# Kernel tuning notes

Measured on AMD Instinct MI355X. Metric: run time of the kernel, lower is better.

Reference implementation:

```python
import jax, jax.numpy as jnp
import numpy as np

N_NODES = 2048
N_EDGES = 32768
NEG_SLOPE = 0.01  # torch F.leaky_relu default used in DGL GAT tutorial


def gat_layer(h, W, a, src, dst):
    """Multi-head GAT layer (DGL tutorial math), concat merge.
    h: [N, F_in], W: [H, F_in, D], a: [H, 2D], src/dst: [E].
    Returns [N, H*D].
    """
    n = h.shape[0]
    D = W.shape[2]
    z = jnp.einsum('ni,hio->nho', h, W)                      # [N,H,D]
    a_src, a_dst = a[:, :D], a[:, D:]
    s_src = jnp.einsum('nhd,hd->nh', z, a_src)               # [N,H]
    s_dst = jnp.einsum('nhd,hd->nh', z, a_dst)               # [N,H]
    e = jax.nn.leaky_relu(s_src[src] + s_dst[dst], NEG_SLOPE)  # [E,H]
    # softmax over incoming edges per destination node
    e_max = jax.ops.segment_max(e, dst, num_segments=n)      # [N,H]
    ex = jnp.exp(e - e_max[dst])                             # [E,H]
    denom = jax.ops.segment_sum(ex, dst, num_segments=n)     # [N,H]
    alpha = ex / denom[dst]                                  # [E,H]
    msg = alpha[:, :, None] * z[src]                         # [E,H,D]
    out = jax.ops.segment_sum(msg, dst, num_segments=n)      # [N,H,D]
    return out.reshape(n, -1)


def setup_inputs() -> dict:
    key = jax.random.key(0)
    ks = jax.random.split(key, 12)

    def w(k, h, i, o):
        return jax.random.normal(k, (h, i, o), jnp.float32) / np.float32(np.sqrt(i))

    def av(k, h, o):
        return jax.random.normal(k, (h, 2 * o), jnp.float32) / np.float32(np.sqrt(2 * o))

    feat = jax.random.normal(ks[0], (N_NODES, 512), jnp.float32)
    W1 = w(ks[1], 16, 512, 512);   a1 = av(ks[2], 16, 512)
    W2 = w(ks[3], 16, 8192, 512);  a2 = av(ks[4], 16, 512)
    W3 = w(ks[5], 16, 8192, 512);  a3 = av(ks[6], 16, 512)
    W4 = w(ks[7], 1, 8192, 512);   a4 = av(ks[8], 1, 512)
    src = jax.random.randint(ks[9], (N_EDGES,), 0, N_NODES, jnp.int32)
    # guarantee every node has at least one incoming edge (no empty softmax)
    dst_rand = jax.random.randint(ks[10], (N_EDGES - N_NODES,), 0, N_NODES, jnp.int32)
    dst = jnp.concatenate([jnp.arange(N_NODES, dtype=jnp.int32), dst_rand])
    return dict(feat=feat, W1=W1, a1=a1, W2=W2, a2=a2, W3=W3, a3=a3,
                W4=W4, a4=a4, src=src, dst=dst)


def reference(feat, W1, a1, W2, a2, W3, a3, W4, a4, src, dst):
    x = gat_layer(feat, W1, a1, src, dst)   # [N, 8192]
    x = gat_layer(x, W2, a2, src, dst)      # [N, 8192]
    x = gat_layer(x, W3, a3, src, dst)      # [N, 8192]
    x = gat_layer(x, W4, a4, src, dst)      # [N, 512]
    return x
```

## Files before the change

kernel.cpp:

```cpp
#include <hip/hip_runtime.h>
#include <hip/hip_bf16.h>
#include <stdint.h>

#define N_NODES 2048
#define N_EDGES 32768

using short8  = __attribute__((ext_vector_type(8))) short;
using floatx4 = __attribute__((ext_vector_type(4))) float;

__device__ __forceinline__ unsigned short f2bf(float f) {
  unsigned u = __float_as_uint(f);
  unsigned r = (u + 0x7fffu + ((u >> 16) & 1u)) >> 16;
  return (unsigned short)r;
}
__device__ __forceinline__ float wave_sum(float v) {
  #pragma unroll
  for (int o = 32; o > 0; o >>= 1) v += __shfl_xor(v, o);
  return v;
}
__device__ __forceinline__ float wave_max(float v) {
  #pragma unroll
  for (int o = 32; o > 0; o >>= 1) v = fmaxf(v, __shfl_xor(v, o));
  return v;
}

__global__ __launch_bounds__(256) void cast_feat(
    const float* __restrict__ in, unsigned short* __restrict__ out, int n4)
{
  int i = blockIdx.x * 256 + threadIdx.x;
  if (i < n4) {
    float4 v = ((const float4*)in)[i];
    ushort4 o;
    o.x = f2bf(v.x); o.y = f2bf(v.y); o.z = f2bf(v.z); o.w = f2bf(v.w);
    ((ushort4*)out)[i] = o;
  }
}

__global__ __launch_bounds__(256) void transpose_w(
    const float* __restrict__ W, unsigned short* __restrict__ Wt, int Fin)
{
  __shared__ unsigned short tile[64][68];
  const int h  = blockIdx.z;
  const int k0 = blockIdx.x * 64;
  const int d0 = blockIdx.y * 64;
  const int t  = threadIdx.x;
  const float*    Wh  = W  + (size_t)h * Fin * 512;
  unsigned short* Wth = Wt + (size_t)h * 512 * Fin;

  const int dl = (t & 15) * 4;
  const int kr = t >> 4;
  #pragma unroll
  for (int p = 0; p < 4; ++p) {
    int k = kr + p * 16;
    float4 v = *(const float4*)(Wh + (size_t)(k0 + k) * 512 + d0 + dl);
    ushort4 b;
    b.x = f2bf(v.x); b.y = f2bf(v.y); b.z = f2bf(v.z); b.w = f2bf(v.w);
    *(ushort4*)&tile[k][dl] = b;
  }
  __syncthreads();
  const int kl = (t & 15) * 4;
  const int dr = t >> 4;
  #pragma unroll
  for (int p = 0; p < 4; ++p) {
    int d = dr + p * 16;
    ushort4 v;
    v.x = tile[kl + 0][d];
    v.y = tile[kl + 1][d];
    v.z = tile[kl + 2][d];
    v.w = tile[kl + 3][d];
    *(ushort4*)(Wth + (size_t)(d0 + d) * Fin + k0 + kl) = v;
  }
}

#define GLDS(g, l) __builtin_amdgcn_global_load_lds(                       \
    (const __attribute__((address_space(1))) void*)(g),                    \
    (__attribute__((address_space(3))) void*)(l), 16, 0, 0)

__global__ __launch_bounds__(512, 2) void gemm8(
    const unsigned short* __restrict__ A,
    const unsigned short* __restrict__ Bt,
    float* __restrict__ C, int K, int ldc, int colbase)
{
  __shared__ __align__(16) unsigned short lds_buf[4][16384];

  const int tid  = threadIdx.x;
  const int w    = tid >> 6;
  const int lane = tid & 63;
  const int l16  = lane & 15;
  const int quad = lane >> 4;
  const int warp_m = w >> 2;
  const int warp_n = w & 3;

  const int nwg = gridDim.x;
  const int cpx = nwg >> 3;
  const int wg  = (blockIdx.x & 7) * cpx + (blockIdx.x >> 3);
  const int mt  = wg & 7;
  const int nt  = wg >> 3;

  const int NT = K >> 5;

  const int srow = lane >> 2;
  const int gch  = ((lane & 3) ^ ((lane >> 3) & 3)) * 8;
  const unsigned short* pa0 = A  + (size_t)(mt * 256 + w * 32 + srow) * K + gch;
  const unsigned short* pa1 = pa0 + (size_t)16 * K;
  const unsigned short* pb0 = Bt + (size_t)(nt * 256 + w * 32 + srow) * K + gch;
  const unsigned short* pb1 = pb0 + (size_t)16 * K;

  const int fA   = (l16 >> 1) & 3;
  const int cswz = (quad ^ fA) * 8;
  const int a_off = (warp_m * 128 + l16) * 32 + cswz;
  const int b_off = 8192 + (warp_n * 64 + l16) * 32 + cswz;

  floatx4 acc[8][4];
  #pragma unroll
  for (int i = 0; i < 8; ++i)
    #pragma unroll
    for (int j = 0; j < 4; ++j)
      acc[i][j] = (floatx4){0.f, 0.f, 0.f, 0.f};

  {
    unsigned short* dA0 = &lds_buf[0][w * 1024];
    unsigned short* dB0 = &lds_buf[0][8192 + w * 1024];
    GLDS(pa0, dA0); GLDS(pa1, dA0 + 512);
    GLDS(pb0, dB0); GLDS(pb1, dB0 + 512);
    unsigned short* dA1 = &lds_buf[1][w * 1024];
    unsigned short* dB1 = &lds_buf[1][8192 + w * 1024];
    GLDS(pa0 + 32, dA1); GLDS(pa1 + 32, dA1 + 512);
    GLDS(pb0 + 32, dB1); GLDS(pb1 + 32, dB1 + 512);
  }
  asm volatile("s_waitcnt vmcnt(4)");
  __builtin_amdgcn_s_barrier();
  __builtin_amdgcn_sched_barrier(0);

  const unsigned short* sa0 = pa0 + 64;
  const unsigned short* sa1 = pa1 + 64;
  const unsigned short* sb0 = pb0 + 64;
  const unsigned short* sb1 = pb1 + 64;

  for (int t = 0; t < NT; ++t) {
    const int s  = t & 3;
    const int s2 = (t + 2) & 3;
    const unsigned short* sl  = &lds_buf[s][0];
    const unsigned short* rdA = sl + a_off;
    const unsigned short* rdB = sl + b_off;
    const bool st = (t + 2) < NT;

    short8 af[4], bf4[4];
    #pragma unroll
    for (int mi = 0; mi < 4; ++mi)
      af[mi] = *(const short8*)(rdA + mi * 512);
    #pragma unroll
    for (int ni = 0; ni < 4; ++ni)
      bf4[ni] = *(const short8*)(rdB + ni * 512);
    if (st) {
      unsigned short* dA = &lds_buf[s2][w * 1024];
      GLDS(sa0, dA); GLDS(sa1, dA + 512);
    }
    __builtin_amdgcn_sched_barrier(0);
    __builtin_amdgcn_s_barrier();
    asm volatile("s_waitcnt lgkmcnt(0)");
    __builtin_amdgcn_sched_barrier(0);
    __builtin_amdgcn_s_setprio(1);
    #pragma unroll
    for (int mi = 0; mi < 4; ++mi)
      #pragma unroll
      for (int ni = 0; ni < 4; ++ni)
        acc[mi][ni] = __builtin_amdgcn_mfma_f32_16x16x32_bf16(
            af[mi], bf4[ni], acc[mi][ni], 0, 0, 0);
    __builtin_amdgcn_s_setprio(0);
    __builtin_amdgcn_sched_barrier(0);
    __builtin_amdgcn_s_barrier();
    __builtin_amdgcn_sched_barrier(0);

    short8 ag[4];
    #pragma unroll
    for (int mi = 0; mi < 4; ++mi)
      ag[mi] = *(const short8*)(rdA + (mi + 4) * 512);
    if (st) {
      unsigned short* dB = &lds_buf[s2][8192 + w * 1024];
      GLDS(sb0, dB); GLDS(sb1, dB + 512);
    }
    __builtin_amdgcn_sched_barrier(0);
    __builtin_amdgcn_s_barrier();
    asm volatile("s_waitcnt lgkmcnt(0)");
    __builtin_amdgcn_sched_barrier(0);
    __builtin_amdgcn_s_setprio(1);
    #pragma unroll
    for (int mi = 0; mi < 4; ++mi)
      #pragma unroll
      for (int ni = 0; ni < 4; ++ni)
        acc[mi + 4][ni] = __builtin_amdgcn_mfma_f32_16x16x32_bf16(
            ag[mi], bf4[ni], acc[mi + 4][ni], 0, 0, 0);
    __builtin_amdgcn_s_setprio(0);
    __builtin_amdgcn_sched_barrier(0);
    if (st) asm volatile("s_waitcnt vmcnt(4)");
    else    asm volatile("s_waitcnt vmcnt(0)");
    __builtin_amdgcn_s_barrier();
    __builtin_amdgcn_sched_barrier(0);

    sa0 += 32; sa1 += 32; sb0 += 32; sb1 += 32;
  }

  float* Cb = C + (size_t)(mt * 256 + warp_m * 128) * ldc
                + colbase + nt * 256 + warp_n * 64;
  #pragma unroll
  for (int mi = 0; mi < 8; ++mi)
    #pragma unroll
    for (int ni = 0; ni < 4; ++ni)
      #pragma unroll
      for (int r = 0; r < 4; ++r) {
        int row = mi * 16 + quad * 4 + r;
        int col = ni * 16 + l16;
        Cb[(size_t)row * ldc + col] = acc[mi][ni][r];
      }
}

__global__ __launch_bounds__(256) void gemm_bt(
    const unsigned short* __restrict__ A,
    const unsigned short* __restrict__ Bt,
    float* __restrict__ C, int K, int HD, int h0, int klen)
{
  __shared__ unsigned short As[128 * 32];
  __shared__ unsigned short Bs[128 * 32];
  const int tid  = threadIdx.x;
  const int w    = tid >> 6;
  const int lane = tid & 63;
  const int mt   = blockIdx.x;
  const int nt   = blockIdx.y;
  const int hloc = nt >> 2;
  const int nloc = (nt & 3) << 7;
  const int kstart = blockIdx.z * klen;

  const unsigned short* Ab = A  + (size_t)mt * 128 * K;
  const unsigned short* Bb = Bt + (size_t)hloc * 512 * K + (size_t)nloc * K;

  const int srow = lane >> 2;
  const int scol = (lane & 3) << 3;
  const unsigned short* ga = Ab + (size_t)(w * 32 + srow) * K + scol + kstart;
  const unsigned short* gb = Bb + (size_t)(w * 32 + srow) * K + scol + kstart;

  floatx4 acc[4][4];
  #pragma unroll
  for (int i = 0; i < 4; ++i)
    #pragma unroll
    for (int j = 0; j < 4; ++j)
      acc[i][j] = (floatx4){0.f, 0.f, 0.f, 0.f};

  const int quad = lane >> 4;
  const int l16  = lane & 15;
  const int wm   = (w >> 1) << 6;
  const int wn   = (w & 1) << 6;

  for (int kb = 0; kb < klen; kb += 32) {
    __builtin_amdgcn_global_load_lds(
        (const __attribute__((address_space(1))) void*)ga,
        (__attribute__((address_space(3))) void*)&As[w * 1024], 16, 0, 0);
    __builtin_amdgcn_global_load_lds(
        (const __attribute__((address_space(1))) void*)(ga + (size_t)16 * K),
        (__attribute__((address_space(3))) void*)&As[w * 1024 + 512], 16, 0, 0);
    __builtin_amdgcn_global_load_lds(
        (const __attribute__((address_space(1))) void*)gb,
        (__attribute__((address_space(3))) void*)&Bs[w * 1024], 16, 0, 0);
    __builtin_amdgcn_global_load_lds(
        (const __attribute__((address_space(1))) void*)(gb + (size_t)16 * K),
        (__attribute__((address_space(3))) void*)&Bs[w * 1024 + 512], 16, 0, 0);
    ga += 32; gb += 32;
    __syncthreads();

    short8 af[4], bfr[4];
    #pragma unroll
    for (int mi = 0; mi < 4; ++mi)
      af[mi] = *(const short8*)&As[(wm + mi * 16 + l16) * 32 + quad * 8];
    #pragma unroll
    for (int ni = 0; ni < 4; ++ni)
      bfr[ni] = *(const short8*)&Bs[(wn + ni * 16 + l16) * 32 + quad * 8];
    #pragma unroll
    for (int mi = 0; mi < 4; ++mi)
      #pragma unroll
      for (int ni = 0; ni < 4; ++ni)
        acc[mi][ni] = __builtin_amdgcn_mfma_f32_16x16x32_bf16(
            af[mi], bfr[ni], acc[mi][ni], 0, 0, 0);
    __syncthreads();
  }

  float* Cb = C + (size_t)(mt * 128) * HD + (h0 + hloc) * 512 + nloc;
  if (gridDim.z > 1) {
    #pragma unroll
    for (int mi = 0; mi < 4; ++mi)
      #pragma unroll
      for (int ni = 0; ni < 4; ++ni)
        #pragma unroll
        for (int r = 0; r < 4; ++r) {
          int row = wm + mi * 16 + quad * 4 + r;
          int col = wn + ni * 16 + l16;
          atomicAdd(&Cb[(size_t)row * HD + col], acc[mi][ni][r]);
        }
  } else {
    #pragma unroll
    for (int mi = 0; mi < 4; ++mi)
      #pragma unroll
      for (int ni = 0; ni < 4; ++ni)
        #pragma unroll
        for (int r = 0; r < 4; ++r) {
          int row = wm + mi * 16 + quad * 4 + r;
          int col = wn + ni * 16 + l16;
          Cb[(size_t)row * HD + col] = acc[mi][ni][r];
        }
  }
}

__global__ __launch_bounds__(64) void sdot_kernel(
    const float* __restrict__ z, const float* __restrict__ a,
    float* __restrict__ ssrc, float* __restrict__ sdst, int H)
{
  const int idx  = blockIdx.x;
  const int n    = idx / H;
  const int h    = idx % H;
  const int lane = threadIdx.x;
  const float4* zr = (const float4*)(z + (size_t)n * H * 512 + h * 512 + lane * 8);
  float4 z0 = zr[0], z1 = zr[1];
  const float4* as = (const float4*)(a + (size_t)h * 1024 + lane * 8);
  const float4* ad = (const float4*)(a + (size_t)h * 1024 + 512 + lane * 8);
  float4 a0 = as[0], a1 = as[1];
  float4 b0 = ad[0], b1 = ad[1];
  float s1 = z0.x*a0.x + z0.y*a0.y + z0.z*a0.z + z0.w*a0.w
           + z1.x*a1.x + z1.y*a1.y + z1.z*a1.z + z1.w*a1.w;
  float s2 = z0.x*b0.x + z0.y*b0.y + z0.z*b0.z + z0.w*b0.w
           + z1.x*b1.x + z1.y*b1.y + z1.z*b1.z + z1.w*b1.w;
  s1 = wave_sum(s1);
  s2 = wave_sum(s2);
  if (lane == 0) { ssrc[idx] = s1; sdst[idx] = s2; }
}

__global__ void count_k(const int* __restrict__ dst, int* __restrict__ cnt) {
  int e = blockIdx.x * 256 + threadIdx.x;
  if (e < N_EDGES) atomicAdd(&cnt[dst[e]], 1);
}

__global__ __launch_bounds__(256) void scan_k(
    const int* __restrict__ cnt, int* __restrict__ offs, int* __restrict__ cur)
{
  __shared__ int part[256];
  int t = threadIdx.x;
  int loc[8]; int s = 0;
  #pragma unroll
  for (int j = 0; j < 8; ++j) { loc[j] = s; s += cnt[t * 8 + j]; }
  part[t] = s;
  __syncthreads();
  for (int d = 1; d < 256; d <<= 1) {
    int v = (t >= d) ? part[t - d] : 0;
    __syncthreads();
    part[t] += v;
    __syncthreads();
  }
  int base = (t == 0) ? 0 : part[t - 1];
  #pragma unroll
  for (int j = 0; j < 8; ++j) {
    int o = base + loc[j];
    offs[t * 8 + j] = o;
    cur[t * 8 + j]  = o;
  }
  if (t == 255) offs[2048] = part[255];
}

__global__ void scatter_k(const int* __restrict__ dst, const int* __restrict__ srcv,
                          int* __restrict__ cur, int* __restrict__ esrc) {
  int e = blockIdx.x * 256 + threadIdx.x;
  if (e < N_EDGES) {
    int p = atomicAdd(&cur[dst[e]], 1);
    esrc[p] = srcv[e];
  }
}

__global__ __launch_bounds__(64) void attn_agg(
    const float* __restrict__ z, const float* __restrict__ ssrc,
    const float* __restrict__ sdst, const int* __restrict__ offs,
    const int* __restrict__ esrc, unsigned short* __restrict__ outb,
    float* __restrict__ outf, int H)
{
  const int n = blockIdx.x, h = blockIdx.y, lane = threadIdx.x;
  const int s0 = offs[n], s1 = offs[n + 1];
  const float sd = sdst[n * H + h];

  float m = -3e38f;
  for (int i = s0 + lane; i < s1; i += 64) {
    float s = ssrc[esrc[i] * H + h] + sd;
    s = (s > 0.f) ? s : s * 0.01f;
    m = fmaxf(m, s);
  }
  m = wave_max(m);

  float den = 0.f;
  for (int i = s0 + lane; i < s1; i += 64) {
    float s = ssrc[esrc[i] * H + h] + sd;
    s = (s > 0.f) ? s : s * 0.01f;
    den += __expf(s - m);
  }
  den = wave_sum(den);
  const float inv = 1.f / den;

  float acc[8] = {0.f, 0.f, 0.f, 0.f, 0.f, 0.f, 0.f, 0.f};
  const float* zb = z + (size_t)h * 512 + lane * 8;
  for (int i = s0; i < s1; ++i) {
    int se = esrc[i];
    float s = ssrc[se * H + h] + sd;
    s = (s > 0.f) ? s : s * 0.01f;
    float alpha = __expf(s - m) * inv;
    const float4* zr = (const float4*)(zb + (size_t)se * H * 512);
    float4 q0 = zr[0], q1 = zr[1];
    acc[0] += alpha * q0.x; acc[1] += alpha * q0.y;
    acc[2] += alpha * q0.z; acc[3] += alpha * q0.w;
    acc[4] += alpha * q1.x; acc[5] += alpha * q1.y;
    acc[6] += alpha * q1.z; acc[7] += alpha * q1.w;
  }

  const size_t base = (size_t)n * H * 512 + h * 512 + lane * 8;
  if (outf) {
    float4 o0 = {acc[0], acc[1], acc[2], acc[3]};
    float4 o1 = {acc[4], acc[5], acc[6], acc[7]};
    *(float4*)(outf + base)     = o0;
    *(float4*)(outf + base + 4) = o1;
  } else {
    uint4 pk;
    pk.x = (unsigned)f2bf(acc[0]) | ((unsigned)f2bf(acc[1]) << 16);
    pk.y = (unsigned)f2bf(acc[2]) | ((unsigned)f2bf(acc[3]) << 16);
    pk.z = (unsigned)f2bf(acc[4]) | ((unsigned)f2bf(acc[5]) << 16);
    pk.w = (unsigned)f2bf(acc[6]) | ((unsigned)f2bf(acc[7]) << 16);
    *(uint4*)(outb + base) = pk;
  }
}

extern "C" void kernel_launch(void* const* d_in, const int* in_sizes, int n_in,
                              void* d_out, int out_size, void* d_ws, size_t ws_size,
                              hipStream_t stream)
{
  (void)in_sizes; (void)n_in; (void)out_size;
  const float* feat = (const float*)d_in[0];
  const float* W1   = (const float*)d_in[1];
  const float* a1   = (const float*)d_in[2];
  const float* W2   = (const float*)d_in[3];
  const float* a2   = (const float*)d_in[4];
  const float* W3   = (const float*)d_in[5];
  const float* a3   = (const float*)d_in[6];
  const float* W4   = (const float*)d_in[7];
  const float* a4   = (const float*)d_in[8];
  const int* src = (const int*)d_in[9];
  const int* dst = (const int*)d_in[10];
  float* out = (float*)d_out;

  const size_t WT16 = (size_t)16 * 512 * 8192 * 2;
  const size_t WT8  = WT16 / 2;
  const size_t ZSZ  = (size_t)N_NODES * 16 * 512 * 4;
  const size_t XSZ  = (size_t)N_NODES * 8192 * 2;
  const size_t X0SZ = (size_t)N_NODES * 512 * 2;
  const size_t SMALL = 131072 + 131072 + 8192 + 8448 + 8192 + 131072;
  const size_t NEED16 = WT16 + ZSZ + XSZ + X0SZ + SMALL;

  const int ngroups = (ws_size >= NEED16) ? 1 : 2;
  const size_t wtsz = (ngroups == 1) ? WT16 : WT8;

  char* ws = (char*)d_ws;
  unsigned short* wt = (unsigned short*)ws;
  float* z           = (float*)(ws + wtsz);
  unsigned short* x  = (unsigned short*)(ws + wtsz + ZSZ);
  unsigned short* x0 = (unsigned short*)(ws + wtsz + ZSZ + XSZ);
  char* sm           = ws + wtsz + ZSZ + XSZ + X0SZ;
  float* ssrc        = (float*)(sm);
  float* sdst        = (float*)(sm + 131072);
  int* cnt           = (int*)(sm + 262144);
  int* offs          = (int*)(sm + 270336);
  int* cur           = (int*)(sm + 278784);
  int* esrc          = (int*)(sm + 286976);

  hipMemsetAsync(cnt, 0, N_NODES * sizeof(int), stream);
  count_k<<<N_EDGES / 256, 256, 0, stream>>>(dst, cnt);
  scan_k<<<1, 256, 0, stream>>>(cnt, offs, cur);
  scatter_k<<<N_EDGES / 256, 256, 0, stream>>>(dst, src, cur, esrc);

  cast_feat<<<1024, 256, 0, stream>>>(feat, x0, N_NODES * 512 / 4);

  auto run_big = [&](const float* W, const unsigned short* xin, int Fin) {
    const int hpg = 16 / ngroups;
    for (int g = 0; g < ngroups; ++g) {
      transpose_w<<<dim3(Fin / 64, 8, hpg), 256, 0, stream>>>(
          W + (size_t)g * hpg * Fin * 512, wt, Fin);
      const int ntn = hpg * 2;
      gemm8<<<dim3(8 * ntn), 512, 0, stream>>>(
          xin, wt, z, Fin, 8192, g * hpg * 512);
    }
  };

  transpose_w<<<dim3(8, 8, 16), 256, 0, stream>>>(W1, wt, 512);
  gemm8<<<dim3(8 * 32), 512, 0, stream>>>(x0, wt, z, 512, 8192, 0);
  sdot_kernel<<<N_NODES * 16, 64, 0, stream>>>(z, a1, ssrc, sdst, 16);
  attn_agg<<<dim3(N_NODES, 16), 64, 0, stream>>>(z, ssrc, sdst, offs, esrc,
                                                 x, nullptr, 16);

  run_big(W2, x, 8192);
  sdot_kernel<<<N_NODES * 16, 64, 0, stream>>>(z, a2, ssrc, sdst, 16);
  attn_agg<<<dim3(N_NODES, 16), 64, 0, stream>>>(z, ssrc, sdst, offs, esrc,
                                                 x, nullptr, 16);

  run_big(W3, x, 8192);
  sdot_kernel<<<N_NODES * 16, 64, 0, stream>>>(z, a3, ssrc, sdst, 16);
  attn_agg<<<dim3(N_NODES, 16), 64, 0, stream>>>(z, ssrc, sdst, offs, esrc,
                                                 x, nullptr, 16);

  transpose_w<<<dim3(128, 8, 1), 256, 0, stream>>>(W4, wt, 8192);
  hipMemsetAsync(z, 0, (size_t)N_NODES * 512 * sizeof(float), stream);
  gemm_bt<<<dim3(16, 4, 8), 256, 0, stream>>>(x, wt, z, 8192, 512, 0, 1024);
  sdot_kernel<<<N_NODES, 64, 0, stream>>>(z, a4, ssrc, sdst, 1);
  attn_agg<<<dim3(N_NODES, 1), 64, 0, stream>>>(z, ssrc, sdst, offs, esrc,
                                                nullptr, out, 1);
}
```

Measured before the change: 1.540 ms.

## Fuse weight transpose/cast into GEMM B-load and attention dot into epilogue

The GEMM now reads fp32 weights in their original [H,K,D] layout directly from global memory into registers, converts them to bf16 and writes swizzled tiles to LDS, so the separate transpose_w pass and its bf16 workspace copy are no longer needed. The attention score dot products (s_src, s_dst) are computed in the GEMM epilogue with shuffle reductions and atomicAdd, which replaces the sdot_kernel launch and its re-read of z. The trade-off is B loads that go through registers instead of direct global-to-LDS loads, extra VGPR pressure, and atomics that make the score sums order-nondeterministic. Workspace offsets are now hardcoded, and the half-size weight-group fallback for smaller workspaces is dropped.

```diff
diff --git a/kernel.cpp b/kernel.cpp
--- a/kernel.cpp
+++ b/kernel.cpp
@@ -76,10 +76,33 @@
     (const __attribute__((address_space(1))) void*)(g),                    \
     (__attribute__((address_space(3))) void*)(l), 16, 0, 0)
 
+#define LOAD_B(BV, KBASE)                                                  \
+  {                                                                        \
+    _Pragma("unroll")                                                      \
+    for (int j = 0; j < 4; ++j)                                            \
+      *(float4*)((BV)[j]) =                                                \
+          *(const float4*)(bbase + (size_t)((KBASE) + j) * 512);           \
+  }
+
+#define WRITE_B(BV, SLOTPTR)                                               \
+  {                                                                        \
+    _Pragma("unroll")                                                      \
+    for (int i = 0; i < 4; ++i) {                                          \
+      const int row = (nq << 2) + i;                                       \
+      const int sw  = (row >> 1) & 3;                                      \
+      uint2 pk;                                                            \
+      pk.x = (unsigned)f2bf((BV)[0][i]) | ((unsigned)f2bf((BV)[1][i]) << 16); \
+      pk.y = (unsigned)f2bf((BV)[2][i]) | ((unsigned)f2bf((BV)[3][i]) << 16); \
+      *(uint2*)&(SLOTPTR)[row * 32 + ((kc ^ sw) << 3) + ko] = pk;          \
+    }                                                                      \
+  }
+
 __global__ __launch_bounds__(512, 2) void gemm8(
     const unsigned short* __restrict__ A,
-    const unsigned short* __restrict__ Bt,
-    float* __restrict__ C, int K, int ldc, int colbase)
+    const float* __restrict__ Wn,
+    float* __restrict__ C, int K, int ldc,
+    const float* __restrict__ avec,
+    float* __restrict__ ssrc, float* __restrict__ sdst)
 {
   __shared__ __align__(16) unsigned short lds_buf[4][16384];
 
@@ -101,10 +124,17 @@
 
   const int srow = lane >> 2;
   const int gch  = ((lane & 3) ^ ((lane >> 3) & 3)) * 8;
-  const unsigned short* pa0 = A  + (size_t)(mt * 256 + w * 32 + srow) * K + gch;
+  const unsigned short* pa0 = A + (size_t)(mt * 256 + w * 32 + srow) * K + gch;
   const unsigned short* pa1 = pa0 + (size_t)16 * K;
-  const unsigned short* pb0 = Bt + (size_t)(nt * 256 + w * 32 + srow) * K + gch;
-  const unsigned short* pb1 = pb0 + (size_t)16 * K;
+
+  const int h   = nt >> 1;
+  const int nq  = (w << 3) + (lane >> 3);
+  const int kg  = lane & 7;
+  const int kc  = kg >> 1;
+  const int ko  = (kg & 1) << 2;
+  const float* bbase = Wn + (size_t)h * K * 512
+                     + (nt & 1) * 256 + (nq << 2)
+                     + (size_t)(kg << 2) * 512;
 
   const int fA   = (l16 >> 1) & 3;
   const int cswz = (quad ^ fA) * 8;
@@ -119,23 +149,23 @@
       acc[i][j] = (floatx4){0.f, 0.f, 0.f, 0.f};
 
   {
+    float b0v[4][4], b1v[4][4];
+    LOAD_B(b0v, 0);
     unsigned short* dA0 = &lds_buf[0][w * 1024];
-    unsigned short* dB0 = &lds_buf[0][8192 + w * 1024];
     GLDS(pa0, dA0); GLDS(pa1, dA0 + 512);
-    GLDS(pb0, dB0); GLDS(pb1, dB0 + 512);
+    LOAD_B(b1v, 32);
     unsigned short* dA1 = &lds_buf[1][w * 1024];
-    unsigned short* dB1 = &lds_buf[1][8192 + w * 1024];
     GLDS(pa0 + 32, dA1); GLDS(pa1 + 32, dA1 + 512);
-    GLDS(pb0 + 32, dB1); GLDS(pb1 + 32, dB1 + 512);
-  }
-  asm volatile("s_waitcnt vmcnt(4)");
-  __builtin_amdgcn_s_barrier();
-  __builtin_amdgcn_sched_barrier(0);
+    WRITE_B(b0v, &lds_buf[0][8192]);
+    WRITE_B(b1v, &lds_buf[1][8192]);
+    asm volatile("s_waitcnt vmcnt(0)");
+    asm volatile("s_waitcnt lgkmcnt(0)");
+    __builtin_amdgcn_s_barrier();
+    __builtin_amdgcn_sched_barrier(0);
+  }
 
   const unsigned short* sa0 = pa0 + 64;
   const unsigned short* sa1 = pa1 + 64;
-  const unsigned short* sb0 = pb0 + 64;
-  const unsigned short* sb1 = pb1 + 64;
 
   for (int t = 0; t < NT; ++t) {
     const int s  = t & 3;
@@ -152,7 +182,9 @@
     #pragma unroll
     for (int ni = 0; ni < 4; ++ni)
       bf4[ni] = *(const short8*)(rdB + ni * 512);
+    float bv[4][4];
     if (st) {
+      LOAD_B(bv, (t + 2) * 32);
       unsigned short* dA = &lds_buf[s2][w * 1024];
       GLDS(sa0, dA); GLDS(sa1, dA + 512);
     }
@@ -177,8 +209,9 @@
     for (int mi = 0; mi < 4; ++mi)
       ag[mi] = *(const short8*)(rdA + (mi + 4) * 512);
     if (st) {
-      unsigned short* dB = &lds_buf[s2][8192 + w * 1024];
-      GLDS(sb0, dB); GLDS(sb1, dB + 512);
+      asm volatile("s_waitcnt vmcnt(2)");
+      __builtin_amdgcn_sched_barrier(0);
+      WRITE_B(bv, &lds_buf[s2][8192]);
     }
     __builtin_amdgcn_sched_barrier(0);
     __builtin_amdgcn_s_barrier();
@@ -193,16 +226,15 @@
             ag[mi], bf4[ni], acc[mi + 4][ni], 0, 0, 0);
     __builtin_amdgcn_s_setprio(0);
     __builtin_amdgcn_sched_barrier(0);
-    if (st) asm volatile("s_waitcnt vmcnt(4)");
-    else    asm volatile("s_waitcnt vmcnt(0)");
+    if (t == NT - 2) asm volatile("s_waitcnt vmcnt(0)");
     __builtin_amdgcn_s_barrier();
     __builtin_amdgcn_sched_barrier(0);
 
-    sa0 += 32; sa1 += 32; sb0 += 32; sb1 += 32;
+    sa0 += 32; sa1 += 32;
   }
 
   float* Cb = C + (size_t)(mt * 256 + warp_m * 128) * ldc
-                + colbase + nt * 256 + warp_n * 64;
+                + nt * 256 + warp_n * 64;
   #pragma unroll
   for (int mi = 0; mi < 8; ++mi)
     #pragma unroll
@@ -213,6 +245,39 @@
         int col = ni * 16 + l16;
         Cb[(size_t)row * ldc + col] = acc[mi][ni][r];
       }
+
+  if (avec) {
+    const int dbase = (nt & 1) * 256 + warp_n * 64;
+    float asv[4], adv[4];
+    #pragma unroll
+    for (int ni = 0; ni < 4; ++ni) {
+      int d = dbase + ni * 16 + l16;
+      asv[ni] = avec[h * 1024 + d];
+      adv[ni] = avec[h * 1024 + 512 + d];
+    }
+    #pragma unroll
+    for (int mi = 0; mi < 8; ++mi)
+      #pragma unroll
+      for (int r = 0; r < 4; ++r) {
+        float ps = 0.f, pd = 0.f;
+        #pragma unroll
+        for (int ni = 0; ni < 4; ++ni) {
+          float v = acc[mi][ni][r];
+          ps += v * asv[ni];
+          pd += v * adv[ni];
+        }
+        #pragma unroll
+        for (int o = 1; o < 16; o <<= 1) {
+          ps += __shfl_xor(ps, o);
+          pd += __shfl_xor(pd, o);
+        }
+        if (l16 == 0) {
+          int n = mt * 256 + warp_m * 128 + mi * 16 + quad * 4 + r;
+          atomicAdd(&ssrc[n * 16 + h], ps);
+          atomicAdd(&sdst[n * 16 + h], pd);
+        }
+      }
+  }
 }
 
 __global__ __launch_bounds__(256) void gemm_bt(
@@ -434,7 +499,7 @@
                               void* d_out, int out_size, void* d_ws, size_t ws_size,
                               hipStream_t stream)
 {
-  (void)in_sizes; (void)n_in; (void)out_size;
+  (void)in_sizes; (void)n_in; (void)out_size; (void)ws_size;
   const float* feat = (const float*)d_in[0];
   const float* W1   = (const float*)d_in[1];
   const float* a1   = (const float*)d_in[2];
@@ -448,23 +513,12 @@
   const int* dst = (const int*)d_in[10];
   float* out = (float*)d_out;
 
-  const size_t WT16 = (size_t)16 * 512 * 8192 * 2;
-  const size_t WT8  = WT16 / 2;
-  const size_t ZSZ  = (size_t)N_NODES * 16 * 512 * 4;
-  const size_t XSZ  = (size_t)N_NODES * 8192 * 2;
-  const size_t X0SZ = (size_t)N_NODES * 512 * 2;
-  const size_t SMALL = 131072 + 131072 + 8192 + 8448 + 8192 + 131072;
-  const size_t NEED16 = WT16 + ZSZ + XSZ + X0SZ + SMALL;
-
-  const int ngroups = (ws_size >= NEED16) ? 1 : 2;
-  const size_t wtsz = (ngroups == 1) ? WT16 : WT8;
-
   char* ws = (char*)d_ws;
   unsigned short* wt = (unsigned short*)ws;
-  float* z           = (float*)(ws + wtsz);
-  unsigned short* x  = (unsigned short*)(ws + wtsz + ZSZ);
-  unsigned short* x0 = (unsigned short*)(ws + wtsz + ZSZ + XSZ);
-  char* sm           = ws + wtsz + ZSZ + XSZ + X0SZ;
+  float* z           = (float*)(ws + 16777216);
+  unsigned short* x  = (unsigned short*)(ws + 83886080);
+  unsigned short* x0 = (unsigned short*)(ws + 117440512);
+  char* sm           = ws + 119537664;
   float* ssrc        = (float*)(sm);
   float* sdst        = (float*)(sm + 131072);
   int* cnt           = (int*)(sm + 262144);
@@ -479,32 +533,18 @@
 
   cast_feat<<<1024, 256, 0, stream>>>(feat, x0, N_NODES * 512 / 4);
 
-  auto run_big = [&](const float* W, const unsigned short* xin, int Fin) {
-    const int hpg = 16 / ngroups;
-    for (int g = 0; g < ngroups; ++g) {
-      transpose_w<<<dim3(Fin / 64, 8, hpg), 256, 0, stream>>>(
-          W + (size_t)g * hpg * Fin * 512, wt, Fin);
-      const int ntn = hpg * 2;
-      gemm8<<<dim3(8 * ntn), 512, 0, stream>>>(
-          xin, wt, z, Fin, 8192, g * hpg * 512);
-    }
+  auto layer16 = [&](const float* W, const float* av,
+                     const unsigned short* xin, int Fin,
+                     unsigned short* xout) {
+    hipMemsetAsync(ssrc, 0, 2 * N_NODES * 16 * sizeof(float), stream);
+    gemm8<<<dim3(256), 512, 0, stream>>>(xin, W, z, Fin, 8192, av, ssrc, sdst);
+    attn_agg<<<dim3(N_NODES, 16), 64, 0, stream>>>(z, ssrc, sdst, offs, esrc,
+                                                   xout, nullptr, 16);
   };
 
-  transpose_w<<<dim3(8, 8, 16), 256, 0, stream>>>(W1, wt, 512);
-  gemm8<<<dim3(8 * 32), 512, 0, stream>>>(x0, wt, z, 512, 8192, 0);
-  sdot_kernel<<<N_NODES * 16, 64, 0, stream>>>(z, a1, ssrc, sdst, 16);
-  attn_agg<<<dim3(N_NODES, 16), 64, 0, stream>>>(z, ssrc, sdst, offs, esrc,
-                                                 x, nullptr, 16);
-
-  run_big(W2, x, 8192);
-  sdot_kernel<<<N_NODES * 16, 64, 0, stream>>>(z, a2, ssrc, sdst, 16);
-  attn_agg<<<dim3(N_NODES, 16), 64, 0, stream>>>(z, ssrc, sdst, offs, esrc,
-                                                 x, nullptr, 16);
-
-  run_big(W3, x, 8192);
-  sdot_kernel<<<N_NODES * 16, 64, 0, stream>>>(z, a3, ssrc, sdst, 16);
-  attn_agg<<<dim3(N_NODES, 16), 64, 0, stream>>>(z, ssrc, sdst, offs, esrc,
-                                                 x, nullptr, 16);
+  layer16(W1, a1, x0, 512, x);
+  layer16(W2, a2, x, 8192, x);
+  layer16(W3, a3, x, 8192, x);
 
   transpose_w<<<dim3(128, 8, 1), 256, 0, stream>>>(W4, wt, 8192);
   hipMemsetAsync(z, 0, (size_t)N_NODES * 512 * sizeof(float), stream);
```

Measured after the change: 2.184 ms. +41.9%, slower.
